# Kernel tuning notes

Hardware: AMD Instinct MI355X
Metric: run time of the kernel (lower is better)

Reference implementation:

```python
import jax, jax.numpy as jnp
import numpy as np

D = 512
B, S1, S2 = 8, 2048, 2048


def setup_inputs() -> dict:
    key = jax.random.key(0)
    ks = jax.random.split(key, 8)
    s = 1.0 / np.sqrt(D)
    return {
        "x1": jax.random.normal(ks[0], (B, S1, D), dtype=jnp.float32),
        "x2": jax.random.normal(ks[1], (B, S2, D), dtype=jnp.float32),
        "Wq": jax.random.normal(ks[2], (D, D), dtype=jnp.float32) * s,
        "bq": jnp.zeros((D,), dtype=jnp.float32),
        "Wk": jax.random.normal(ks[3], (D, D), dtype=jnp.float32) * s,
        "bk": jnp.zeros((D,), dtype=jnp.float32),
        "Wv": jax.random.normal(ks[4], (D, D), dtype=jnp.float32) * s,
        "bv": jnp.zeros((D,), dtype=jnp.float32),
    }


def reference(x1, x2, Wq, bq, Wk, bk, Wv, bv):
    # q,k,v projections (torch Linear: x @ W^T + b)
    q = jnp.einsum("bsd,ed->bse", x1, Wq) + bq  # [B,S1,D]
    k = jnp.einsum("btd,ed->bte", x2, Wk) + bk  # [B,S2,D]
    v = jnp.einsum("btd,ed->bte", x2, Wv) + bv  # [B,S2,D]
    # NOTE: source scales by input_dim (D), not sqrt(D)
    scores = jnp.einsum("bse,bte->bst", q, k) / D  # [B,S1,S2]
    attn = jax.nn.softmax(scores, axis=-1)
    return jnp.einsum("bst,bte->bse", attn, v)  # [B,S1,D]
```

## Files before the change

kernel.cpp:

```cpp
#include <hip/hip_runtime.h>

using u8  = unsigned char;
using u16 = unsigned short;
using u32 = unsigned int;
using s16x8 = __attribute__((ext_vector_type(8))) short;
using bf16x8 = __attribute__((ext_vector_type(8))) __bf16;
using f32x4 = __attribute__((ext_vector_type(4))) float;
using i32x4 = __attribute__((ext_vector_type(4))) int;
using i32x8 = __attribute__((ext_vector_type(8))) int;

__device__ inline u16 f2bf(float f) {
  u32 u = __float_as_uint(f);
  u = (u + 0x7FFFu + ((u >> 16) & 1u)) >> 16;
  return (u16)u;
}

__device__ inline u8 f2fp8(float f) {
  return (u8)(__builtin_amdgcn_cvt_pk_fp8_f32(f, f, 0, false) & 0xFF);
}

__device__ inline f32x4 mfma16(s16x8 a, s16x8 b, f32x4 c) {
  return __builtin_amdgcn_mfma_f32_16x16x32_bf16(
      __builtin_bit_cast(bf16x8, a), __builtin_bit_cast(bf16x8, b), c, 0, 0, 0);
}

__device__ inline f32x4 mfma_fp8(i32x8 a, i32x8 b, f32x4 c) {
  return __builtin_amdgcn_mfma_scale_f32_16x16x128_f8f6f4(
      a, b, c, 0 , 0 , 0, 127, 0, 127);
}

__device__ inline void load_lds16(const void* g, void* l) {
  __builtin_amdgcn_global_load_lds(
      (const __attribute__((address_space(1))) void*)g,
      (__attribute__((address_space(3))) void*)l, 16, 0, 0);
}

__global__ __launch_bounds__(256) void cast_all(
    const float* __restrict__ x1, const float* __restrict__ x2,
    const float* __restrict__ wq, const float* __restrict__ wk,
    const float* __restrict__ wv, u16* __restrict__ o1, u16* __restrict__ o2,
    u16* __restrict__ oq, u16* __restrict__ ok, u16* __restrict__ ov) {
  const float* in;
  u16* out;
  int bx = blockIdx.x;
  if (blockIdx.y == 0) {
    in = x1; out = o1;
  } else if (blockIdx.y == 1) {
    in = x2; out = o2;
  } else {
    if (bx >= 768) return;
    const int w = bx >> 8;
    in = w == 0 ? wq : (w == 1 ? wk : wv);
    out = w == 0 ? oq : (w == 1 ? ok : ov);
    bx &= 255;
  }
  int i = (bx * 256 + threadIdx.x) * 4;
  float4 f = *(const float4*)(in + i);
  ushort4 o;
  o.x = f2bf(f.x); o.y = f2bf(f.y); o.z = f2bf(f.z); o.w = f2bf(f.w);
  *(ushort4*)(out + i) = o;
}

__global__ __launch_bounds__(256) void gemm_proj(
    const u16* __restrict__ x1b, const u16* __restrict__ x2b,
    const u16* __restrict__ Wqb, const u16* __restrict__ Wkb,
    const u16* __restrict__ Wvb, u8* __restrict__ qb8, u8* __restrict__ kb8,
    u16* __restrict__ vTb, const float* __restrict__ bq,
    const float* __restrict__ bk, const float* __restrict__ bv) {
  int flat = blockIdx.x + 12 * blockIdx.y;
  flat = (flat & 7) * 192 + (flat >> 3);
  const int col = flat % 12;
  const int m0 = (flat / 12) * 128;

  const u16* Ax; const u16* Bw; const float* bias; int n0w, mode;
  if (col < 4)      { Ax = x1b; Bw = Wqb; bias = bq; n0w = col * 128;       mode = 0; }
  else if (col < 8) { Ax = x2b; Bw = Wkb; bias = bk; n0w = (col - 4) * 128; mode = 1; }
  else              { Ax = x2b; Bw = Wvb; bias = bv; n0w = (col - 8) * 128; mode = 2; }

  const int tid = threadIdx.x;
  const int lane = tid & 63;
  const int wave = tid >> 6;
  const int wm = (wave >> 1) * 64;
  const int wn = (wave & 1) * 64;

  __shared__ u16 As_[2][128 * 64];
  __shared__ u16 Bs_[2][128 * 64];

  const int sr = lane >> 3;
  const int gd = (lane & 7) ^ sr;
  const int fr = lane & 15;
  const int fg = lane >> 4;

  auto stage = [&](int k0, int b) {
#pragma unroll
    for (int it = 0; it < 4; ++it) {
      const int ch = wave * 4 + it;
      const int row = ch * 8 + sr;
      load_lds16(Ax + (size_t)(m0 + row) * 512 + k0 + gd * 8, &As_[b][ch * 512]);
      load_lds16(Bw + (size_t)(n0w + row) * 512 + k0 + gd * 8, &Bs_[b][ch * 512]);
    }
  };

  f32x4 acc[4][4];
#pragma unroll
  for (int i = 0; i < 4; ++i)
#pragma unroll
    for (int j = 0; j < 4; ++j) acc[i][j] = 0.0f;

  stage(0, 0);
  __syncthreads();

  for (int ks = 0; ks < 8; ++ks) {
    const int b = ks & 1;
    if (ks < 7) stage((ks + 1) * 64, b ^ 1);
#pragma unroll
    for (int s = 0; s < 2; ++s) {
      const int slot = ((s * 4 + fg) ^ (fr & 7)) * 8;
      s16x8 af[4], bfr[4];
#pragma unroll
      for (int i = 0; i < 4; ++i) {
        af[i]  = *(const s16x8*)&As_[b][(wm + i * 16 + fr) * 64 + slot];
        bfr[i] = *(const s16x8*)&Bs_[b][(wn + i * 16 + fr) * 64 + slot];
      }
      __builtin_amdgcn_s_setprio(1);
#pragma unroll
      for (int mi = 0; mi < 4; ++mi)
#pragma unroll
        for (int ni = 0; ni < 4; ++ni)
          acc[mi][ni] = mfma16(af[mi], bfr[ni], acc[mi][ni]);
      __builtin_amdgcn_s_setprio(0);
    }
    __syncthreads();
  }

  const int er = fg * 4;
  const int ec = fr;

  if (mode != 2) {
    u8* Cb = (mode == 0) ? qb8 : kb8;
#pragma unroll
    for (int mi = 0; mi < 4; ++mi)
#pragma unroll
      for (int ni = 0; ni < 4; ++ni) {
        const int colg = n0w + wn + ni * 16 + ec;
        const float badd = bias[colg];
#pragma unroll
        for (int i = 0; i < 4; ++i) {
          const int row = m0 + wm + mi * 16 + er + i;
          Cb[(size_t)row * 512 + colg] = f2fp8(acc[mi][ni][i] + badd);
        }
      }
  } else {
    u16* Tb = &As_[0][0];
    const int batch = m0 >> 11;
    const int srow = m0 & 2047;
    u16* Cv = vTb + (size_t)batch * (512 * 2048);
#pragma unroll
    for (int h = 0; h < 2; ++h) {
      if ((wn >> 6) == h) {
#pragma unroll
        for (int mi = 0; mi < 4; ++mi)
#pragma unroll
          for (int ni = 0; ni < 4; ++ni) {
            const int c = ni * 16 + ec;
            const float badd = bias[n0w + wn + c];
#pragma unroll
            for (int i = 0; i < 4; ++i) {
              const int r = wm + mi * 16 + er + i;
              Tb[c * 136 + r] = f2bf(acc[mi][ni][i] + badd);
            }
          }
      }
      __syncthreads();
      const int d = tid >> 2;
      const int sc = (tid & 3) * 32;
      const int dglob = n0w + 64 * h + d;
#pragma unroll
      for (int j = 0; j < 4; ++j) {
        uint4 v = *(const uint4*)&Tb[d * 136 + sc + j * 8];
        *(uint4*)&Cv[(size_t)dglob * 2048 + srow + sc + j * 8] = v;
      }
      __syncthreads();
    }
  }
}

__global__ __launch_bounds__(512, 2) void attn_fused(
    const u8* __restrict__ q8, const u8* __restrict__ k8,
    const u16* __restrict__ vT, float* __restrict__ out) {
  const int batch = blockIdx.x;
  const int q0 = blockIdx.y * 64;
  const u8* qb = q8 + ((size_t)batch * 2048 + q0) * 512;
  const u8* kb = k8 + (size_t)batch * 2048 * 512;
  const u16* vb = vT + (size_t)batch * 512 * 2048;
  float* ob = out + ((size_t)batch * 2048 + q0) * 512;

  const int tid = threadIdx.x;
  const int lane = tid & 63;
  const int wave = tid >> 6;
  const int wm = (wave >> 1) * 16;
  const int wn = (wave & 1) * 32;
  const int wd = wave * 64;
  const int sr = lane >> 3;
  const int gd = (lane & 7) ^ sr;
  const int fr = lane & 15;
  const int fg = lane >> 4;
  const int r7 = fr & 7;
  const int s0 = (2 * fg) ^ r7;
  const int s1 = s0 ^ 1;

  __shared__ u8 Ks[2][4][8192];
  __shared__ u16 Ps[2][64 * 64];

  i32x8 Qf[4];
#pragma unroll
  for (int kc = 0; kc < 4; ++kc) {
    const u8* p = qb + (size_t)(wm + fr) * 512 + kc * 128 + fg * 32;
    i32x4 lo = *(const i32x4*)p;
    i32x4 hi = *(const i32x4*)(p + 16);
    i32x8 q;
    q[0] = lo[0]; q[1] = lo[1]; q[2] = lo[2]; q[3] = lo[3];
    q[4] = hi[0]; q[5] = hi[1]; q[6] = hi[2]; q[7] = hi[3];
    Qf[kc] = q;
  }

  auto stageK = [&](int kv0, int buf) {
#pragma unroll
    for (int it = 0; it < 4; ++it) {
      const int idx = wave * 4 + it;
      const int kc = idx >> 3, sub = idx & 7;
      load_lds16(kb + (size_t)(kv0 + sub * 8 + sr) * 512 + kc * 128 + gd * 16,
                 &Ks[buf][kc][sub * 1024]);
    }
  };
  s16x8 Vr[8];
  auto loadV = [&](int kv0) {
#pragma unroll
    for (int ks = 0; ks < 2; ++ks)
#pragma unroll
      for (int ni = 0; ni < 4; ++ni)
        Vr[ks * 4 + ni] = *(const s16x8*)&vb[(size_t)(wd + ni * 16 + fr) * 2048 +
                                             kv0 + ks * 32 + fg * 8];
  };

  f32x4 oacc[4][4];
#pragma unroll
  for (int i = 0; i < 4; ++i)
#pragma unroll
    for (int j = 0; j < 4; ++j) oacc[i][j] = 0.0f;
  float l_reg[4] = {0.0f, 0.0f, 0.0f, 0.0f};

  constexpr int NT = 32;

  auto tile = [&](int t, int psel) {
    f32x4 sacc[2];
    sacc[0] = 0.0f; sacc[1] = 0.0f;
    __builtin_amdgcn_s_setprio(1);
#pragma unroll
    for (int kc = 0; kc < 4; ++kc) {
#pragma unroll
      for (int ni = 0; ni < 2; ++ni) {
        const u8* pb = &Ks[psel][kc][(wn + ni * 16 + fr) * 128];
        i32x4 blo = *(const i32x4*)(pb + s0 * 16);
        i32x4 bhi = *(const i32x4*)(pb + s1 * 16);
        i32x8 bK;
        bK[0] = blo[0]; bK[1] = blo[1]; bK[2] = blo[2]; bK[3] = blo[3];
        bK[4] = bhi[0]; bK[5] = bhi[1]; bK[6] = bhi[2]; bK[7] = bhi[3];
        sacc[ni] = mfma_fp8(Qf[kc], bK, sacc[ni]);
      }
    }
    __builtin_amdgcn_s_setprio(0);
    u16* Pd = &Ps[psel][0];
#pragma unroll
    for (int ni = 0; ni < 2; ++ni) {
      const int g = (wn >> 3) + ni * 2 + (fr >> 3);
      const int co = fr & 7;
#pragma unroll
      for (int i = 0; i < 4; ++i) {
        const int r = wm + fg * 4 + i;
        const int ph = ((r >> 2) & 1) * 4 + ((r ^ (r >> 3)) & 1) * 2 +
                       ((r >> 1) & 1);
        const float p = __expf(sacc[ni][i] * (1.0f / 512.0f));
        l_reg[i] += p;
        Pd[r * 64 + ((g ^ ph) << 3) + co] = f2bf(p);
      }
    }
    asm volatile("s_waitcnt vmcnt(8) lgkmcnt(0)" ::: "memory");
    __builtin_amdgcn_s_barrier();
    __builtin_amdgcn_sched_barrier(0);
    if (t + 2 < NT) stageK((t + 2) * 64, psel);
    __builtin_amdgcn_sched_barrier(0);
#pragma unroll
    for (int ks = 0; ks < 2; ++ks) {
      s16x8 pa[4];
#pragma unroll
      for (int mi = 0; mi < 4; ++mi) {
        const int r = mi * 16 + fr;
        const int ph = ((r >> 2) & 1) * 4 + ((r ^ (r >> 3)) & 1) * 2 +
                       ((r >> 1) & 1);
        pa[mi] = *(const s16x8*)&Pd[r * 64 + (((ks * 4 + fg) ^ ph) << 3)];
      }
      __builtin_amdgcn_s_setprio(1);
#pragma unroll
      for (int ni = 0; ni < 4; ++ni)
#pragma unroll
        for (int mi = 0; mi < 4; ++mi)
          oacc[mi][ni] = mfma16(pa[mi], Vr[ks * 4 + ni], oacc[mi][ni]);
      __builtin_amdgcn_s_setprio(0);
    }
    if (t + 1 < NT) loadV((t + 1) * 64);
  };

  stageK(0, 0);
  stageK(64, 1);
  __builtin_amdgcn_sched_barrier(0);
  loadV(0);
  asm volatile("s_waitcnt vmcnt(8)" ::: "memory");
  __builtin_amdgcn_s_barrier();
  __builtin_amdgcn_sched_barrier(0);

  for (int tt = 0; tt < NT; tt += 2) {
    tile(tt, 0);
    tile(tt + 1, 1);
  }

  float* lsc = (float*)&Ps[0][0];
  __syncthreads();
#pragma unroll
  for (int i = 0; i < 4; ++i) {
    float rs = l_reg[i];
    rs += __shfl_xor(rs, 1);
    rs += __shfl_xor(rs, 2);
    rs += __shfl_xor(rs, 4);
    rs += __shfl_xor(rs, 8);
    if (fr == 0) lsc[(wn >> 5) * 64 + wm + fg * 4 + i] = rs;
  }
  __syncthreads();

#pragma unroll
  for (int mi = 0; mi < 4; ++mi)
#pragma unroll
    for (int i = 0; i < 4; ++i) {
      const int r = mi * 16 + fg * 4 + i;
      const float l = lsc[r] + lsc[64 + r];
      const float li = __builtin_amdgcn_rcpf(l);
#pragma unroll
      for (int ni = 0; ni < 4; ++ni)
        ob[(size_t)r * 512 + wd + ni * 16 + fr] = oacc[mi][ni][i] * li;
    }
}

extern "C" void kernel_launch(void* const* d_in, const int* in_sizes, int n_in,
                              void* d_out, int out_size, void* d_ws, size_t ws_size,
                              hipStream_t stream) {
  constexpr int B = 8, S = 2048, D = 512;
  constexpr size_t MS = (size_t)B * S;

  const float* x1 = (const float*)d_in[0];
  const float* x2 = (const float*)d_in[1];
  const float* Wq = (const float*)d_in[2];
  const float* bq = (const float*)d_in[3];
  const float* Wk = (const float*)d_in[4];
  const float* bk = (const float*)d_in[5];
  const float* Wv = (const float*)d_in[6];
  const float* bv = (const float*)d_in[7];
  float* out = (float*)d_out;

  u16* x1b = (u16*)d_ws;
  u16* x2b = x1b + MS * D;
  u16* Wqb = x2b + MS * D;
  u16* Wkb = Wqb + (size_t)D * D;
  u16* Wvb = Wkb + (size_t)D * D;
  u16* vTb = Wvb + (size_t)D * D;
  u16* Sc  = vTb + MS * D;
  float* lbuf = (float*)(Sc + (size_t)B * S * S);
  u8* qb8 = (u8*)(lbuf + MS);
  u8* kb8 = qb8 + MS * D;

  dim3 blk(256);

  cast_all<<<dim3((MS * D) / 1024, 3), blk, 0, stream>>>(
      x1, x2, Wq, Wk, Wv, x1b, x2b, Wqb, Wkb, Wvb);

  gemm_proj<<<dim3(12, 128), blk, 0, stream>>>(
      x1b, x2b, Wqb, Wkb, Wvb, qb8, kb8, vTb, bq, bk, bv);

  attn_fused<<<dim3(8, 32, 1), dim3(512), 0, stream>>>(qb8, kb8, vTb, out);
}
```

Before: 254.2 us.

## Fuse fp32-to-bf16 cast into projection GEMM and software-pipeline attention loop

Removes the separate cast kernel. The projection GEMM now loads fp32 inputs and weights into registers, converts them with packed bf16 conversion instructions, and writes them to LDS itself, so the bf16 copies no longer take an extra round trip through global memory. Separately, the attention loop is restructured so the QK^T and exp of the next tile are issued alongside the PV of the current tile, with K staged earlier, to overlap matrix and vector work. This adds register pressure and replaces asynchronous direct-to-LDS loads with a synchronous register path. The s_setprio hints are dropped.

New measurement: 270.7 us. 1.07x slower.

```diff
diff --git a/kernel.cpp b/kernel.cpp
--- a/kernel.cpp
+++ b/kernel.cpp
@@ -35,36 +35,21 @@
       (__attribute__((address_space(3))) void*)l, 16, 0, 0);
 }
 
-__global__ __launch_bounds__(256) void cast_all(
+__device__ inline s16x8 cvt8(f32x4 lo, f32x4 hi) {
+  u32 w0, w1, w2, w3;
+  asm("v_cvt_pk_bf16_f32 %0, %1, %2" : "=v"(w0) : "v"(lo[0]), "v"(lo[1]));
+  asm("v_cvt_pk_bf16_f32 %0, %1, %2" : "=v"(w1) : "v"(lo[2]), "v"(lo[3]));
+  asm("v_cvt_pk_bf16_f32 %0, %1, %2" : "=v"(w2) : "v"(hi[0]), "v"(hi[1]));
+  asm("v_cvt_pk_bf16_f32 %0, %1, %2" : "=v"(w3) : "v"(hi[2]), "v"(hi[3]));
+  i32x4 r;
+  r[0] = (int)w0; r[1] = (int)w1; r[2] = (int)w2; r[3] = (int)w3;
+  return __builtin_bit_cast(s16x8, r);
+}
+
+__global__ __launch_bounds__(256) void gemm_proj(
     const float* __restrict__ x1, const float* __restrict__ x2,
-    const float* __restrict__ wq, const float* __restrict__ wk,
-    const float* __restrict__ wv, u16* __restrict__ o1, u16* __restrict__ o2,
-    u16* __restrict__ oq, u16* __restrict__ ok, u16* __restrict__ ov) {
-  const float* in;
-  u16* out;
-  int bx = blockIdx.x;
-  if (blockIdx.y == 0) {
-    in = x1; out = o1;
-  } else if (blockIdx.y == 1) {
-    in = x2; out = o2;
-  } else {
-    if (bx >= 768) return;
-    const int w = bx >> 8;
-    in = w == 0 ? wq : (w == 1 ? wk : wv);
-    out = w == 0 ? oq : (w == 1 ? ok : ov);
-    bx &= 255;
-  }
-  int i = (bx * 256 + threadIdx.x) * 4;
-  float4 f = *(const float4*)(in + i);
-  ushort4 o;
-  o.x = f2bf(f.x); o.y = f2bf(f.y); o.z = f2bf(f.z); o.w = f2bf(f.w);
-  *(ushort4*)(out + i) = o;
-}
-
-__global__ __launch_bounds__(256) void gemm_proj(
-    const u16* __restrict__ x1b, const u16* __restrict__ x2b,
-    const u16* __restrict__ Wqb, const u16* __restrict__ Wkb,
-    const u16* __restrict__ Wvb, u8* __restrict__ qb8, u8* __restrict__ kb8,
+    const float* __restrict__ Wq, const float* __restrict__ Wk,
+    const float* __restrict__ Wv, u8* __restrict__ qb8, u8* __restrict__ kb8,
     u16* __restrict__ vTb, const float* __restrict__ bq,
     const float* __restrict__ bk, const float* __restrict__ bv) {
   int flat = blockIdx.x + 12 * blockIdx.y;
@@ -72,10 +57,10 @@
   const int col = flat % 12;
   const int m0 = (flat / 12) * 128;
 
-  const u16* Ax; const u16* Bw; const float* bias; int n0w, mode;
-  if (col < 4)      { Ax = x1b; Bw = Wqb; bias = bq; n0w = col * 128;       mode = 0; }
-  else if (col < 8) { Ax = x2b; Bw = Wkb; bias = bk; n0w = (col - 4) * 128; mode = 1; }
-  else              { Ax = x2b; Bw = Wvb; bias = bv; n0w = (col - 8) * 128; mode = 2; }
+  const float* Ax; const float* Bw; const float* bias; int n0w, mode;
+  if (col < 4)      { Ax = x1; Bw = Wq; bias = bq; n0w = col * 128;       mode = 0; }
+  else if (col < 8) { Ax = x2; Bw = Wk; bias = bk; n0w = (col - 4) * 128; mode = 1; }
+  else              { Ax = x2; Bw = Wv; bias = bv; n0w = (col - 8) * 128; mode = 2; }
 
   const int tid = threadIdx.x;
   const int lane = tid & 63;
@@ -91,13 +76,27 @@
   const int fr = lane & 15;
   const int fg = lane >> 4;
 
-  auto stage = [&](int k0, int b) {
+  f32x4 Ar[4][2], Br[4][2];
+
+  auto stage_issue = [&](int k0) {
 #pragma unroll
     for (int it = 0; it < 4; ++it) {
       const int ch = wave * 4 + it;
       const int row = ch * 8 + sr;
-      load_lds16(Ax + (size_t)(m0 + row) * 512 + k0 + gd * 8, &As_[b][ch * 512]);
-      load_lds16(Bw + (size_t)(n0w + row) * 512 + k0 + gd * 8, &Bs_[b][ch * 512]);
+      const float* pa = Ax + (size_t)(m0 + row) * 512 + k0 + gd * 8;
+      const float* pb = Bw + (size_t)(n0w + row) * 512 + k0 + gd * 8;
+      Ar[it][0] = *(const f32x4*)pa;
+      Ar[it][1] = *(const f32x4*)(pa + 4);
+      Br[it][0] = *(const f32x4*)pb;
+      Br[it][1] = *(const f32x4*)(pb + 4);
+    }
+  };
+  auto stage_write = [&](int b) {
+#pragma unroll
+    for (int it = 0; it < 4; ++it) {
+      const int ch = wave * 4 + it;
+      *(s16x8*)&As_[b][ch * 512 + lane * 8] = cvt8(Ar[it][0], Ar[it][1]);
+      *(s16x8*)&Bs_[b][ch * 512 + lane * 8] = cvt8(Br[it][0], Br[it][1]);
     }
   };
 
@@ -107,12 +106,14 @@
 #pragma unroll
     for (int j = 0; j < 4; ++j) acc[i][j] = 0.0f;
 
-  stage(0, 0);
+  stage_issue(0);
+  asm volatile("s_waitcnt vmcnt(0)" ::: "memory");
+  stage_write(0);
   __syncthreads();
 
   for (int ks = 0; ks < 8; ++ks) {
     const int b = ks & 1;
-    if (ks < 7) stage((ks + 1) * 64, b ^ 1);
+    if (ks < 7) stage_issue((ks + 1) * 64);
 #pragma unroll
     for (int s = 0; s < 2; ++s) {
       const int slot = ((s * 4 + fg) ^ (fr & 7)) * 8;
@@ -122,13 +123,15 @@
         af[i]  = *(const s16x8*)&As_[b][(wm + i * 16 + fr) * 64 + slot];
         bfr[i] = *(const s16x8*)&Bs_[b][(wn + i * 16 + fr) * 64 + slot];
       }
-      __builtin_amdgcn_s_setprio(1);
 #pragma unroll
       for (int mi = 0; mi < 4; ++mi)
 #pragma unroll
         for (int ni = 0; ni < 4; ++ni)
           acc[mi][ni] = mfma16(af[mi], bfr[ni], acc[mi][ni]);
-      __builtin_amdgcn_s_setprio(0);
+    }
+    if (ks < 7) {
+      asm volatile("s_waitcnt vmcnt(0)" ::: "memory");
+      stage_write(b ^ 1);
     }
     __syncthreads();
   }
@@ -252,15 +255,12 @@
 
   constexpr int NT = 32;
 
-  auto tile = [&](int t, int psel) {
-    f32x4 sacc[2];
-    sacc[0] = 0.0f; sacc[1] = 0.0f;
-    __builtin_amdgcn_s_setprio(1);
+  auto qk = [&](int kbuf, f32x4* sacc) {
 #pragma unroll
     for (int kc = 0; kc < 4; ++kc) {
 #pragma unroll
       for (int ni = 0; ni < 2; ++ni) {
-        const u8* pb = &Ks[psel][kc][(wn + ni * 16 + fr) * 128];
+        const u8* pb = &Ks[kbuf][kc][(wn + ni * 16 + fr) * 128];
         i32x4 blo = *(const i32x4*)(pb + s0 * 16);
         i32x4 bhi = *(const i32x4*)(pb + s1 * 16);
         i32x8 bK;
@@ -269,8 +269,9 @@
         sacc[ni] = mfma_fp8(Qf[kc], bK, sacc[ni]);
       }
     }
-    __builtin_amdgcn_s_setprio(0);
-    u16* Pd = &Ps[psel][0];
+  };
+  auto expw = [&](int pbuf, const f32x4* sacc) {
+    u16* Pd = &Ps[pbuf][0];
 #pragma unroll
     for (int ni = 0; ni < 2; ++ni) {
       const int g = (wn >> 3) + ni * 2 + (fr >> 3);
@@ -285,11 +286,9 @@
         Pd[r * 64 + ((g ^ ph) << 3) + co] = f2bf(p);
       }
     }
-    asm volatile("s_waitcnt vmcnt(8) lgkmcnt(0)" ::: "memory");
-    __builtin_amdgcn_s_barrier();
-    __builtin_amdgcn_sched_barrier(0);
-    if (t + 2 < NT) stageK((t + 2) * 64, psel);
-    __builtin_amdgcn_sched_barrier(0);
+  };
+  auto pv = [&](int pbuf) {
+    const u16* Pd = &Ps[pbuf][0];
 #pragma unroll
     for (int ks = 0; ks < 2; ++ks) {
       s16x8 pa[4];
@@ -300,29 +299,51 @@
                        ((r >> 1) & 1);
         pa[mi] = *(const s16x8*)&Pd[r * 64 + (((ks * 4 + fg) ^ ph) << 3)];
       }
-      __builtin_amdgcn_s_setprio(1);
 #pragma unroll
       for (int ni = 0; ni < 4; ++ni)
 #pragma unroll
         for (int mi = 0; mi < 4; ++mi)
           oacc[mi][ni] = mfma16(pa[mi], Vr[ks * 4 + ni], oacc[mi][ni]);
-      __builtin_amdgcn_s_setprio(0);
-    }
-    if (t + 1 < NT) loadV((t + 1) * 64);
+    }
+  };
+
+  auto interval = [&](int t, int psel, bool hasNext, bool hasStage) {
+    if (hasStage) stageK((t + 2) * 64, psel);
+    f32x4 sacc[2];
+    sacc[0] = 0.0f; sacc[1] = 0.0f;
+    if (hasNext) qk(psel ^ 1, sacc);
+    pv(psel);
+    if (hasNext) {
+      expw(psel ^ 1, sacc);
+      loadV((t + 1) * 64);
+      asm volatile("s_waitcnt vmcnt(8) lgkmcnt(0)" ::: "memory");
+      __builtin_amdgcn_s_barrier();
+      __builtin_amdgcn_sched_barrier(0);
+    }
   };
 
   stageK(0, 0);
   stageK(64, 1);
-  __builtin_amdgcn_sched_barrier(0);
   loadV(0);
   asm volatile("s_waitcnt vmcnt(8)" ::: "memory");
   __builtin_amdgcn_s_barrier();
   __builtin_amdgcn_sched_barrier(0);
-
-  for (int tt = 0; tt < NT; tt += 2) {
-    tile(tt, 0);
-    tile(tt + 1, 1);
-  }
+  {
+    f32x4 sacc[2];
+    sacc[0] = 0.0f; sacc[1] = 0.0f;
+    qk(0, sacc);
+    expw(0, sacc);
+  }
+  asm volatile("s_waitcnt lgkmcnt(0)" ::: "memory");
+  __builtin_amdgcn_s_barrier();
+  __builtin_amdgcn_sched_barrier(0);
+
+  for (int tt = 0; tt < NT - 2; tt += 2) {
+    interval(tt, 0, true, true);
+    interval(tt + 1, 1, true, true);
+  }
+  interval(NT - 2, 0, true, false);
+  interval(NT - 1, 1, false, false);
 
   float* lsc = (float*)&Ps[0][0];
   __syncthreads();
@@ -379,11 +400,8 @@
 
   dim3 blk(256);
 
-  cast_all<<<dim3((MS * D) / 1024, 3), blk, 0, stream>>>(
-      x1, x2, Wq, Wk, Wv, x1b, x2b, Wqb, Wkb, Wvb);
-
   gemm_proj<<<dim3(12, 128), blk, 0, stream>>>(
-      x1b, x2b, Wqb, Wkb, Wvb, qb8, kb8, vTb, bq, bk, bv);
+      x1, x2, Wq, Wk, Wv, qb8, kb8, vTb, bq, bk, bv);
 
   attn_fused<<<dim3(8, 32, 1), dim3(512), 0, stream>>>(qb8, kb8, vTb, out);
 }
```
